# Performance work log

Hardware: AMD Instinct MI355X
Metric: run time of the kernel (lower is better)

## Reference

```python
import jax, jax.numpy as jnp
import numpy as np

DIM = 768
NUM_HEADS = 4
HEAD_DIM = DIM // NUM_HEADS
SCALE = HEAD_DIM ** -0.5


def setup_inputs() -> dict:
    key = jax.random.key(0)
    ks = jax.random.split(key, 8)
    B, N = 8, 2048
    q = jax.random.normal(ks[0], (B, N, DIM), dtype=jnp.float32)
    k = jax.random.normal(ks[1], (B, N, DIM), dtype=jnp.float32)
    v = jax.random.normal(ks[2], (B, N, DIM), dtype=jnp.float32)
    s = DIM ** -0.5
    Wq = jax.random.normal(ks[3], (DIM, DIM), dtype=jnp.float32) * s
    Wk = jax.random.normal(ks[4], (DIM, DIM), dtype=jnp.float32) * s
    Wv = jax.random.normal(ks[5], (DIM, DIM), dtype=jnp.float32) * s
    Wp = jax.random.normal(ks[6], (DIM, DIM), dtype=jnp.float32) * s
    bp = jnp.zeros((DIM,), dtype=jnp.float32)
    return {"q": q, "k": k, "v": v, "Wq": Wq, "Wk": Wk, "Wv": Wv, "Wp": Wp, "bp": bp}


def reference(q, k, v, Wq, Wk, Wv, Wp, bp):
    B, Nq, C = q.shape
    Nk = k.shape[1]
    H, D = NUM_HEADS, HEAD_DIM
    # Linear projections (nn.Linear: x @ W.T), split heads -> [B, H, N, D]
    qh = (q @ Wq.T).reshape(B, Nq, H, D).transpose(0, 2, 1, 3)
    kh = (k @ Wk.T).reshape(B, Nk, H, D).transpose(0, 2, 1, 3)
    vh = (v @ Wv.T).reshape(B, Nk, H, D).transpose(0, 2, 1, 3)
    # Attention scores [B, H, Nq, Nk], softmax over keys
    attn = jnp.einsum('bhqd,bhkd->bhqk', qh, kh) * SCALE
    attn = jax.nn.softmax(attn, axis=-1)
    # Weighted values -> merge heads -> output projection
    x = jnp.einsum('bhqk,bhkd->bhqd', attn, vh)
    x = x.transpose(0, 2, 1, 3).reshape(B, Nq, C)
    return x @ Wp.T + bp
```

## Files before the change

### kernel.cpp

```cpp
#include <hip/hip_runtime.h>
#include <hip/hip_fp16.h>

#define DIMC 768
#define NH 4
#define HD 192
#define SEQ 2048
#define NBATCH 8
#define SCALE_F 0.07216878364870323f
#define LOG2E   1.4426950408889634f
#define DEFER_THR 8.0f

typedef _Float16 f16x8 __attribute__((ext_vector_type(8)));
typedef _Float16 f16x4 __attribute__((ext_vector_type(4)));
typedef float    f32x4 __attribute__((ext_vector_type(4)));

__device__ __forceinline__ f32x4 mfma16(f16x8 a, f16x8 b, f32x4 c) {
    return __builtin_amdgcn_mfma_f32_16x16x32_f16(a, b, c, 0, 0, 0);
}
__device__ __forceinline__ void gl16(const void* g, void* l) {
    __builtin_amdgcn_global_load_lds(
        (const __attribute__((address_space(1))) unsigned int*)g,
        (__attribute__((address_space(3))) unsigned int*)l, 16, 0, 0);
}
__device__ __forceinline__ float exp2_hw(float x) {
    return __builtin_amdgcn_exp2f(x);
}

__global__ __launch_bounds__(256)
void cvt_w(const float* __restrict__ w0, const float* __restrict__ w1,
           const float* __restrict__ w2, const float* __restrict__ w3,
           _Float16* __restrict__ o0, _Float16* __restrict__ o1,
           _Float16* __restrict__ o2, _Float16* __restrict__ o3)
{
    const float* src = (blockIdx.y == 0) ? w0 : (blockIdx.y == 1) ? w1
                     : (blockIdx.y == 2) ? w2 : w3;
    _Float16* dst = (blockIdx.y == 0) ? o0 : (blockIdx.y == 1) ? o1
                  : (blockIdx.y == 2) ? o2 : o3;
    const int e   = blockIdx.x * 256 + threadIdx.x;
    const int row = e / 192;
    const int col = (e - row * 192) * 4;
    const float4 v = *(const float4*)(src + (size_t)row * DIMC + col);
    const int nt = row >> 8, rr = row & 255, t = col >> 6, cc = col & 63;
    f16x4 h = {(_Float16)v.x, (_Float16)v.y, (_Float16)v.z, (_Float16)v.w};
    *(f16x4*)(dst + ((size_t)(nt * 12 + t) * 256 + rr) * 64 + (cc ^ ((rr & 7) << 3))) = h;
}

__device__ __forceinline__ void phase_reads(const _Float16* As, const _Float16* Bs,
                                            int wr, int wc, int l15, int l4, int q,
                                            f16x8 af[2][2], f16x8 bf[2][4], bool loadB)
{
    #pragma unroll
    for (int ks = 0; ks < 2; ++ks) {
        const int cb = ks * 32 + l4 * 8;
        #pragma unroll
        for (int mm = 0; mm < 2; ++mm) {
            const int row = wr * 128 + (q * 2 + mm) * 16 + l15;
            af[ks][mm] = *(const f16x8*)(As + (size_t)row * 64 + (cb ^ ((row & 7) << 3)));
        }
        if (loadB) {
            #pragma unroll
            for (int n = 0; n < 4; ++n) {
                const int row = wc * 64 + n * 16 + l15;
                bf[ks][n] = *(const f16x8*)(Bs + (size_t)row * 64 + (cb ^ ((row & 7) << 3)));
            }
        }
    }
}
__device__ __forceinline__ void phase_mfma(int q, f16x8 af[2][2], f16x8 bf[2][4],
                                           f32x4 acc[8][4])
{
    __builtin_amdgcn_s_barrier();
    asm volatile("s_waitcnt lgkmcnt(0)" ::: "memory");
    __builtin_amdgcn_s_setprio(1);
    #pragma unroll
    for (int ks = 0; ks < 2; ++ks)
        #pragma unroll
        for (int mm = 0; mm < 2; ++mm)
            #pragma unroll
            for (int n = 0; n < 4; ++n)
                acc[q * 2 + mm][n] = mfma16(af[ks][mm], bf[ks][n], acc[q * 2 + mm][n]);
    __builtin_amdgcn_s_setprio(0);
}

template<int MODE>
__global__ __launch_bounds__(512, 2)
void gemm_p8(const float* __restrict__ A, const _Float16* __restrict__ Wimg,
             _Float16* __restrict__ Y, float scale)
{
    __shared__ __attribute__((aligned(16))) _Float16 Abuf[2][16384];
    __shared__ __attribute__((aligned(16))) _Float16 Bbuf[2][16384];

    const int tid  = threadIdx.x;
    const int wid  = tid >> 6;
    const int lane = tid & 63;
    const int l15  = lane & 15;
    const int l4   = lane >> 4;
    const int wr   = wid >> 2;
    const int wc   = wid & 3;
    const int m0   = blockIdx.x * 256;
    const int nt   = blockIdx.y;

    const unsigned char* Wt = (const unsigned char*)(Wimg + (size_t)nt * 12 * 16384);

    f32x4 acc[8][4];
    #pragma unroll
    for (int m = 0; m < 8; ++m)
        #pragma unroll
        for (int n = 0; n < 4; ++n)
            acc[m][n] = (f32x4){0.f, 0.f, 0.f, 0.f};

    float4 rA[8];
    auto loadA = [&](int t) {
        #pragma unroll
        for (int p = 0; p < 8; ++p) {
            const int linear = p * 512 + tid;
            const int row = linear >> 4, qc = (linear & 15) * 4;
            rA[p] = *(const float4*)(A + (size_t)(m0 + row) * DIMC + t * 64 + qc);
        }
    };
    auto writeA = [&](int buf) {
        #pragma unroll
        for (int p = 0; p < 8; ++p) {
            const int linear = p * 512 + tid;
            const int row = linear >> 4, qc = (linear & 15) * 4;
            f16x4 h = {(_Float16)rA[p].x, (_Float16)rA[p].y,
                       (_Float16)rA[p].z, (_Float16)rA[p].w};
            *(f16x4*)(&Abuf[buf][row * 64 + (qc ^ ((row & 7) << 3))]) = h;
        }
    };
    auto stageB = [&](int t) {
        const unsigned char* src = Wt + (size_t)t * 32768;
        #pragma unroll
        for (int u = 0; u < 4; ++u)
            gl16(src + u * 8192 + tid * 16, &Bbuf[t & 1][u * 4096 + tid * 8]);
    };

    loadA(0);
    stageB(0);
    asm volatile("s_waitcnt vmcnt(4)" ::: "memory");
    writeA(0);
    loadA(1);
    asm volatile("s_waitcnt vmcnt(8)" ::: "memory");
    asm volatile("s_waitcnt lgkmcnt(0)" ::: "memory");
    __builtin_amdgcn_s_barrier();

    for (int t = 0; t < 12; ++t) {
        const _Float16* As = &Abuf[t & 1][0];
        const _Float16* Bs = &Bbuf[t & 1][0];
        f16x8 af[2][2], bf[2][4];

        phase_reads(As, Bs, wr, wc, l15, l4, 0, af, bf, true);
        if (t < 11) stageB(t + 1);
        phase_mfma(0, af, bf, acc);
        __builtin_amdgcn_s_barrier();

        phase_reads(As, Bs, wr, wc, l15, l4, 1, af, bf, false);
        phase_mfma(1, af, bf, acc);
        __builtin_amdgcn_s_barrier();

        phase_reads(As, Bs, wr, wc, l15, l4, 2, af, bf, false);
        if (t < 11) {
            asm volatile("s_waitcnt vmcnt(4)" ::: "memory");
            writeA((t + 1) & 1);
            if (t < 10) loadA(t + 2);
        }
        phase_mfma(2, af, bf, acc);
        __builtin_amdgcn_s_barrier();

        phase_reads(As, Bs, wr, wc, l15, l4, 3, af, bf, false);
        phase_mfma(3, af, bf, acc);
        if (t < 10)      asm volatile("s_waitcnt vmcnt(8)" ::: "memory");
        else if (t == 10) asm volatile("s_waitcnt vmcnt(0)" ::: "memory");
        __builtin_amdgcn_s_barrier();
    }

    #pragma unroll
    for (int m = 0; m < 8; ++m) {
        const int rbase = m0 + wr * 128 + m * 16 + l4 * 4;
        #pragma unroll
        for (int n = 0; n < 4; ++n) {
            const int c = nt * 256 + wc * 64 + n * 16 + l15;
            const int h = c / HD;
            const int d = c - h * HD;
            #pragma unroll
            for (int j = 0; j < 4; ++j) {
                const int r  = rbase + j;
                const int b  = r >> 11;
                const int nn = r & (SEQ - 1);
                size_t idx;
                if (MODE == 0) {
                    idx = ((size_t)(b * NH + h) * SEQ + nn) * HD + d;
                } else {
                    const int kt  = nn >> 5;
                    const int key = nn & 31;
                    const size_t tb = ((size_t)(b * NH + h) * 64 + kt) * 12288;
                    if (MODE == 1)
                        idx = tb + (size_t)key * HD + (d ^ ((key & 7) << 3));
                    else
                        idx = tb + 6144 + (((size_t)(key >> 3) * 192 + d) << 3) + (key & 7);
                }
                Y[idx] = (_Float16)(acc[m][n][j] * scale);
            }
        }
    }
}

__global__ __launch_bounds__(512, 2)
void gemm_x8(const _Float16* __restrict__ Ximg, const _Float16* __restrict__ Wimg,
             float* __restrict__ out, const float* __restrict__ bias)
{
    __shared__ __attribute__((aligned(16))) _Float16 Abuf[2][16384];
    __shared__ __attribute__((aligned(16))) _Float16 Bbuf[2][16384];

    const int tid  = threadIdx.x;
    const int wid  = tid >> 6;
    const int lane = tid & 63;
    const int l15  = lane & 15;
    const int l4   = lane >> 4;
    const int wr   = wid >> 2;
    const int wc   = wid & 3;
    const int mt   = blockIdx.x;
    const int nt   = blockIdx.y;

    const unsigned char* Xt = (const unsigned char*)(Ximg + (size_t)mt * 12 * 16384);
    const unsigned char* Wt = (const unsigned char*)(Wimg + (size_t)nt * 12 * 16384);

    f32x4 acc[8][4];
    #pragma unroll
    for (int m = 0; m < 8; ++m)
        #pragma unroll
        for (int n = 0; n < 4; ++n)
            acc[m][n] = (f32x4){0.f, 0.f, 0.f, 0.f};

    auto stageAB = [&](int t) {
        const unsigned char* sa = Xt + (size_t)t * 32768;
        const unsigned char* sb = Wt + (size_t)t * 32768;
        #pragma unroll
        for (int u = 0; u < 4; ++u) {
            gl16(sa + u * 8192 + tid * 16, &Abuf[t & 1][u * 4096 + tid * 8]);
            gl16(sb + u * 8192 + tid * 16, &Bbuf[t & 1][u * 4096 + tid * 8]);
        }
    };

    stageAB(0);
    asm volatile("s_waitcnt vmcnt(0)" ::: "memory");
    __builtin_amdgcn_s_barrier();

    for (int t = 0; t < 12; ++t) {
        const _Float16* As = &Abuf[t & 1][0];
        const _Float16* Bs = &Bbuf[t & 1][0];
        f16x8 af[2][2], bf[2][4];

        phase_reads(As, Bs, wr, wc, l15, l4, 0, af, bf, true);
        if (t < 11) stageAB(t + 1);
        phase_mfma(0, af, bf, acc);
        __builtin_amdgcn_s_barrier();

        phase_reads(As, Bs, wr, wc, l15, l4, 1, af, bf, false);
        phase_mfma(1, af, bf, acc);
        __builtin_amdgcn_s_barrier();

        phase_reads(As, Bs, wr, wc, l15, l4, 2, af, bf, false);
        phase_mfma(2, af, bf, acc);
        __builtin_amdgcn_s_barrier();

        phase_reads(As, Bs, wr, wc, l15, l4, 3, af, bf, false);
        phase_mfma(3, af, bf, acc);
        if (t < 11) asm volatile("s_waitcnt vmcnt(0)" ::: "memory");
        __builtin_amdgcn_s_barrier();
    }

    #pragma unroll
    for (int m = 0; m < 8; ++m) {
        const int rbase = mt * 256 + wr * 128 + m * 16 + l4 * 4;
        #pragma unroll
        for (int n = 0; n < 4; ++n) {
            const int c = nt * 256 + wc * 64 + n * 16 + l15;
            const float bv = bias[c];
            #pragma unroll
            for (int j = 0; j < 4; ++j)
                out[(size_t)(rbase + j) * DIMC + c] = acc[m][n][j] + bv;
        }
    }
}

__global__ __launch_bounds__(512, 4)
void attn7(const _Float16* __restrict__ Qh, const _Float16* __restrict__ KVimg,
           _Float16* __restrict__ Ximg)
{
    __shared__ __attribute__((aligned(16))) _Float16 KV[2][12288];
    __shared__ __attribute__((aligned(16))) _Float16 Ps[8][16][40];

    const int tid  = threadIdx.x;
    const int wid  = tid >> 6;
    const int lane = tid & 63;
    const int l15  = lane & 15;
    const int l4   = lane >> 4;

    const int bid   = blockIdx.x;
    const int local = bid >> 3;
    const int bh    = (bid & 7) * 4 + (local >> 4);
    const int qt    = local & 15;

    const unsigned char* KVt = (const unsigned char*)KVimg + (size_t)bh * 64 * 24576;

    #pragma unroll
    for (int s = 0; s < 3; ++s)
        gl16(KVt + (size_t)(s * 512 + tid) * 16, &KV[0][(size_t)(s * 512 + tid) * 8]);

    const int q0 = qt * 128 + wid * 16;
    const size_t qbase = (size_t)bh * SEQ * HD;
    f16x8 qf[6];
    #pragma unroll
    for (int kk = 0; kk < 6; ++kk)
        qf[kk] = *(const f16x8*)(Qh + qbase + (size_t)(q0 + l15) * HD + kk * 32 + l4 * 8);

    f32x4 Oacc[12];
    #pragma unroll
    for (int nd = 0; nd < 12; ++nd)
        Oacc[nd] = (f32x4){0.f, 0.f, 0.f, 0.f};
    float mrow[4], lrow[4];
    #pragma unroll
    for (int j = 0; j < 4; ++j) { mrow[j] = -1e30f; lrow[j] = 0.f; }

    for (int kt = 0; kt < SEQ / 32; ++kt) {
        const int cur = kt & 1;
        if (kt < SEQ / 32 - 1) {
            const unsigned char* KVn = KVt + (size_t)(kt + 1) * 24576;
            #pragma unroll
            for (int s = 0; s < 3; ++s)
                gl16(KVn + (size_t)(s * 512 + tid) * 16,
                     &KV[cur ^ 1][(size_t)(s * 512 + tid) * 8]);
            asm volatile("s_waitcnt vmcnt(3)" ::: "memory");
        } else {
            asm volatile("s_waitcnt vmcnt(0)" ::: "memory");
        }
        __builtin_amdgcn_s_barrier();
        __builtin_amdgcn_sched_barrier(0);

        const _Float16* Kc = &KV[cur][0];
        const _Float16* Vc = &KV[cur][6144];

        f32x4 sacc[2];
        sacc[0] = (f32x4){0.f, 0.f, 0.f, 0.f};
        sacc[1] = (f32x4){0.f, 0.f, 0.f, 0.f};
        __builtin_amdgcn_s_setprio(1);
        #pragma unroll
        for (int kk = 0; kk < 6; ++kk) {
            const int cb = (kk * 32 + l4 * 8) ^ ((l15 & 7) << 3);
            #pragma unroll
            for (int nn = 0; nn < 2; ++nn) {
                const f16x8 kf = *(const f16x8*)(Kc + (size_t)(nn * 16 + l15) * HD + cb);
                sacc[nn] = mfma16(qf[kk], kf, sacc[nn]);
            }
        }
        __builtin_amdgcn_s_setprio(0);

        float lm[4];
        bool need = false;
        #pragma unroll
        for (int j = 0; j < 4; ++j) {
            lm[j] = fmaxf(sacc[0][j], sacc[1][j]);
            need |= (lm[j] > mrow[j] + DEFER_THR);
        }
        if (__any(need)) {
            #pragma unroll
            for (int j = 0; j < 4; ++j) {
                float v = lm[j];
                v = fmaxf(v, __shfl_xor(v, 1));
                v = fmaxf(v, __shfl_xor(v, 2));
                v = fmaxf(v, __shfl_xor(v, 4));
                v = fmaxf(v, __shfl_xor(v, 8));
                const float mnew = fmaxf(mrow[j], v);
                const float f    = exp2_hw(mrow[j] - mnew);
                mrow[j] = mnew;
                lrow[j] *= f;
                #pragma unroll
                for (int nd = 0; nd < 12; ++nd)
                    Oacc[nd][j] *= f;
            }
        }
        #pragma unroll
        for (int j = 0; j < 4; ++j) {
            const float p0 = exp2_hw(sacc[0][j] - mrow[j]);
            const float p1 = exp2_hw(sacc[1][j] - mrow[j]);
            sacc[0][j] = p0;
            sacc[1][j] = p1;
            lrow[j] += p0 + p1;
        }

        #pragma unroll
        for (int nn = 0; nn < 2; ++nn)
            #pragma unroll
            for (int j = 0; j < 4; ++j)
                Ps[wid][l4 * 4 + j][nn * 16 + l15] = (_Float16)sacc[nn][j];
        asm volatile("s_waitcnt lgkmcnt(0)" ::: "memory");
        __builtin_amdgcn_sched_barrier(0);

        const f16x8 pf = *(const f16x8*)(&Ps[wid][l15][l4 * 8]);
        __builtin_amdgcn_s_setprio(1);
        #pragma unroll
        for (int nd = 0; nd < 12; ++nd) {
            const f16x8 vfr = *(const f16x8*)(Vc + (((size_t)l4 * 192 + nd * 16 + l15) << 3));
            Oacc[nd] = mfma16(pf, vfr, Oacc[nd]);
        }
        __builtin_amdgcn_s_setprio(0);

        __builtin_amdgcn_s_barrier();
        __builtin_amdgcn_sched_barrier(0);
    }

    #pragma unroll
    for (int j = 0; j < 4; ++j) {
        float s = lrow[j];
        s += __shfl_xor(s, 1);
        s += __shfl_xor(s, 2);
        s += __shfl_xor(s, 4);
        s += __shfl_xor(s, 8);
        lrow[j] = s;
    }
    const int b = bh >> 2;
    const int h = bh & 3;
    #pragma unroll
    for (int j = 0; j < 4; ++j) {
        const float inv = 1.f / lrow[j];
        const int qrow = q0 + l4 * 4 + j;
        const int gr   = b * SEQ + qrow;
        const int mt   = gr >> 8;
        const int rr   = gr & 255;
        #pragma unroll
        for (int nd = 0; nd < 12; ++nd) {
            const int gc = h * HD + nd * 16 + l15;
            const int t  = gc >> 6;
            const int cc = gc & 63;
            Ximg[((size_t)(mt * 12 + t) * 256 + rr) * 64 + (cc ^ ((rr & 7) << 3))] =
                (_Float16)(Oacc[nd][j] * inv);
        }
    }
}

extern "C" void kernel_launch(void* const* d_in, const int* in_sizes, int n_in,
                              void* d_out, int out_size, void* d_ws, size_t ws_size,
                              hipStream_t stream)
{
    const float* q  = (const float*)d_in[0];
    const float* k  = (const float*)d_in[1];
    const float* v  = (const float*)d_in[2];
    const float* Wq = (const float*)d_in[3];
    const float* Wk = (const float*)d_in[4];
    const float* Wv = (const float*)d_in[5];
    const float* Wp = (const float*)d_in[6];
    const float* bp = (const float*)d_in[7];

    const size_t HSZ  = (size_t)NBATCH * NH * SEQ * HD;
    const size_t WIMG = 3 * 12 * 16384;
    _Float16* Qh    = (_Float16*)d_ws;
    _Float16* KVimg = Qh + HSZ;
    _Float16* Ximg  = KVimg + 2 * HSZ;
    _Float16* Wpimg = Ximg + HSZ;
    _Float16* Wqimg = (_Float16*)d_out;
    _Float16* Wkimg = Wqimg + WIMG;
    _Float16* Wvimg = Wkimg + WIMG;

    cvt_w<<<dim3(576, 4), dim3(256), 0, stream>>>(Wq, Wk, Wv, Wp,
                                                  Wqimg, Wkimg, Wvimg, Wpimg);
    dim3 g8(64, 3), b8(512);
    gemm_p8<0><<<g8, b8, 0, stream>>>(q, Wqimg, Qh, SCALE_F * LOG2E);
    gemm_p8<1><<<g8, b8, 0, stream>>>(k, Wkimg, KVimg, 1.0f);
    gemm_p8<3><<<g8, b8, 0, stream>>>(v, Wvimg, KVimg, 1.0f);
    attn7<<<dim3(512), dim3(512), 0, stream>>>(Qh, KVimg, Ximg);
    gemm_x8<<<g8, b8, 0, stream>>>(Ximg, Wpimg, (float*)d_out, bp);
}
```

Before: 262.8 us.

## Merge Q/K/V projection GEMMs into one launch and unroll attention K/V double buffer

Replaces three separate projection GEMM launches with a single 64x9 grid kernel that picks the q/k/v input, weight slice and output layout from blockIdx.y. This gives one larger wave of blocks that can fill the GPU better and removes two launch gaps and their tails. The attention kernel now splits the K/V double buffer into two named LDS arrays and unrolls the tile loop by two, so buffer addresses are static instead of computed from kt&1. The merged kernel adds runtime branches in the epilogue, and a leftover unused gemm_qkv kernel is also added.

```diff
diff --git a/kernel.cpp b/kernel.cpp
--- a/kernel.cpp
+++ b/kernel.cpp
@@ -82,10 +82,9 @@
     __builtin_amdgcn_s_setprio(0);
 }
 
-template<int MODE>
 __global__ __launch_bounds__(512, 2)
-void gemm_p8(const float* __restrict__ A, const _Float16* __restrict__ Wimg,
-             _Float16* __restrict__ Y, float scale)
+void gemm_qkv(const float* __restrict__ A, const _Float16* __restrict__ Wimg,
+              _Float16* __restrict__ Qh, _Float16* __restrict__ KVimg, float qs)
 {
     __shared__ __attribute__((aligned(16))) _Float16 Abuf[2][16384];
     __shared__ __attribute__((aligned(16))) _Float16 Bbuf[2][16384];
@@ -99,6 +98,9 @@
     const int wc   = wid & 3;
     const int m0   = blockIdx.x * 256;
     const int nt   = blockIdx.y;
+    const int which = nt / 3;
+    const int sub   = nt - which * 3;
+    const float scale = (which == 0) ? qs : 1.0f;
 
     const unsigned char* Wt = (const unsigned char*)(Wimg + (size_t)nt * 12 * 16384);
 
@@ -108,6 +110,8 @@
         #pragma unroll
         for (int n = 0; n < 4; ++n)
             acc[m][n] = (f32x4){0.f, 0.f, 0.f, 0.f};
+
+    const float* Asrc = A + (size_t)which * (16384ull * DIMC);
 
     float4 rA[8];
     auto loadA = [&](int t) {
@@ -115,7 +119,7 @@
         for (int p = 0; p < 8; ++p) {
             const int linear = p * 512 + tid;
             const int row = linear >> 4, qc = (linear & 15) * 4;
-            rA[p] = *(const float4*)(A + (size_t)(m0 + row) * DIMC + t * 64 + qc);
+            rA[p] = *(const float4*)(Asrc + (size_t)(m0 + row) * DIMC + t * 64 + qc);
         }
     };
     auto writeA = [&](int buf) {
@@ -169,7 +173,7 @@
 
         phase_reads(As, Bs, wr, wc, l15, l4, 3, af, bf, false);
         phase_mfma(3, af, bf, acc);
-        if (t < 10)      asm volatile("s_waitcnt vmcnt(8)" ::: "memory");
+        if (t < 10)       asm volatile("s_waitcnt vmcnt(8)" ::: "memory");
         else if (t == 10) asm volatile("s_waitcnt vmcnt(0)" ::: "memory");
         __builtin_amdgcn_s_barrier();
     }
@@ -179,7 +183,7 @@
         const int rbase = m0 + wr * 128 + m * 16 + l4 * 4;
         #pragma unroll
         for (int n = 0; n < 4; ++n) {
-            const int c = nt * 256 + wc * 64 + n * 16 + l15;
+            const int c = sub * 256 + wc * 64 + n * 16 + l15;
             const int h = c / HD;
             const int d = c - h * HD;
             #pragma unroll
@@ -187,19 +191,20 @@
                 const int r  = rbase + j;
                 const int b  = r >> 11;
                 const int nn = r & (SEQ - 1);
-                size_t idx;
-                if (MODE == 0) {
-                    idx = ((size_t)(b * NH + h) * SEQ + nn) * HD + d;
+                if (which == 0) {
+                    Qh[((size_t)(b * NH + h) * SEQ + nn) * HD + d] =
+                        (_Float16)(acc[m][n][j] * scale);
                 } else {
                     const int kt  = nn >> 5;
                     const int key = nn & 31;
                     const size_t tb = ((size_t)(b * NH + h) * 64 + kt) * 12288;
-                    if (MODE == 1)
+                    size_t idx;
+                    if (which == 1)
                         idx = tb + (size_t)key * HD + (d ^ ((key & 7) << 3));
                     else
                         idx = tb + 6144 + (((size_t)(key >> 3) * 192 + d) << 3) + (key & 7);
+                    KVimg[idx] = (_Float16)acc[m][n][j];
                 }
-                Y[idx] = (_Float16)(acc[m][n][j] * scale);
             }
         }
     }
@@ -285,10 +290,11 @@
 }
 
 __global__ __launch_bounds__(512, 4)
-void attn7(const _Float16* __restrict__ Qh, const _Float16* __restrict__ KVimg,
+void attn8(const _Float16* __restrict__ Qh, const _Float16* __restrict__ KVimg,
            _Float16* __restrict__ Ximg)
 {
-    __shared__ __attribute__((aligned(16))) _Float16 KV[2][12288];
+    __shared__ __attribute__((aligned(16))) _Float16 KV0[12288];
+    __shared__ __attribute__((aligned(16))) _Float16 KV1[12288];
     __shared__ __attribute__((aligned(16))) _Float16 Ps[8][16][40];
 
     const int tid  = threadIdx.x;
@@ -304,9 +310,14 @@
 
     const unsigned char* KVt = (const unsigned char*)KVimg + (size_t)bh * 64 * 24576;
 
-    #pragma unroll
-    for (int s = 0; s < 3; ++s)
-        gl16(KVt + (size_t)(s * 512 + tid) * 16, &KV[0][(size_t)(s * 512 + tid) * 8]);
+    auto stage = [&](_Float16* dst, int t) {
+        const unsigned char* src = KVt + (size_t)t * 24576;
+        #pragma unroll
+        for (int s = 0; s < 3; ++s)
+            gl16(src + (size_t)(s * 512 + tid) * 16, dst + (size_t)(s * 512 + tid) * 8);
+    };
+
+    stage(KV0, 0);
 
     const int q0 = qt * 128 + wid * 16;
     const size_t qbase = (size_t)bh * SEQ * HD;
@@ -323,23 +334,16 @@
     #pragma unroll
     for (int j = 0; j < 4; ++j) { mrow[j] = -1e30f; lrow[j] = 0.f; }
 
-    for (int kt = 0; kt < SEQ / 32; ++kt) {
-        const int cur = kt & 1;
-        if (kt < SEQ / 32 - 1) {
-            const unsigned char* KVn = KVt + (size_t)(kt + 1) * 24576;
-            #pragma unroll
-            for (int s = 0; s < 3; ++s)
-                gl16(KVn + (size_t)(s * 512 + tid) * 16,
-                     &KV[cur ^ 1][(size_t)(s * 512 + tid) * 8]);
+    auto iter = [&](const _Float16* Kc, const _Float16* Vc,
+                    _Float16* stageDst, int nextT, bool doStage) {
+        if (doStage) {
+            stage(stageDst, nextT);
             asm volatile("s_waitcnt vmcnt(3)" ::: "memory");
         } else {
             asm volatile("s_waitcnt vmcnt(0)" ::: "memory");
         }
         __builtin_amdgcn_s_barrier();
         __builtin_amdgcn_sched_barrier(0);
-
-        const _Float16* Kc = &KV[cur][0];
-        const _Float16* Vc = &KV[cur][6144];
 
         f32x4 sacc[2];
         sacc[0] = (f32x4){0.f, 0.f, 0.f, 0.f};
@@ -408,6 +412,11 @@
 
         __builtin_amdgcn_s_barrier();
         __builtin_amdgcn_sched_barrier(0);
+    };
+
+    for (int kt = 0; kt < SEQ / 32; kt += 2) {
+        iter(&KV0[0], &KV0[6144], KV1, kt + 1, true);
+        iter(&KV1[0], &KV1[6144], KV0, kt + 2, kt + 2 < SEQ / 32);
     }
 
     #pragma unroll
@@ -464,10 +473,141 @@
 
     cvt_w<<<dim3(576, 4), dim3(256), 0, stream>>>(Wq, Wk, Wv, Wp,
                                                   Wqimg, Wkimg, Wvimg, Wpimg);
-    dim3 g8(64, 3), b8(512);
-    gemm_p8<0><<<g8, b8, 0, stream>>>(q, Wqimg, Qh, SCALE_F * LOG2E);
-    gemm_p8<1><<<g8, b8, 0, stream>>>(k, Wkimg, KVimg, 1.0f);
-    gemm_p8<3><<<g8, b8, 0, stream>>>(v, Wvimg, KVimg, 1.0f);
-    attn7<<<dim3(512), dim3(512), 0, stream>>>(Qh, KVimg, Ximg);
-    gemm_x8<<<g8, b8, 0, stream>>>(Ximg, Wpimg, (float*)d_out, bp);
-}
+    (void)0;
+    {
+        extern __global__ void gemm_qkv3(const float*, const float*, const float*,
+                                         const _Float16*, _Float16*, _Float16*, float);
+        gemm_qkv3<<<dim3(64, 9), dim3(512), 0, stream>>>(q, k, v, Wqimg, Qh, KVimg,
+                                                         SCALE_F * LOG2E);
+    }
+    attn8<<<dim3(512), dim3(512), 0, stream>>>(Qh, KVimg, Ximg);
+    gemm_x8<<<dim3(64, 3), dim3(512), 0, stream>>>(Ximg, Wpimg, (float*)d_out, bp);
+}
+
+__global__ __launch_bounds__(512, 2)
+void gemm_qkv3(const float* __restrict__ qA, const float* __restrict__ kA,
+               const float* __restrict__ vA, const _Float16* __restrict__ Wimg,
+               _Float16* __restrict__ Qh, _Float16* __restrict__ KVimg, float qs)
+{
+    __shared__ __attribute__((aligned(16))) _Float16 Abuf[2][16384];
+    __shared__ __attribute__((aligned(16))) _Float16 Bbuf[2][16384];
+
+    const int tid  = threadIdx.x;
+    const int wid  = tid >> 6;
+    const int lane = tid & 63;
+    const int l15  = lane & 15;
+    const int l4   = lane >> 4;
+    const int wr   = wid >> 2;
+    const int wc   = wid & 3;
+    const int m0   = blockIdx.x * 256;
+    const int nt   = blockIdx.y;
+    const int which = nt / 3;
+    const int sub   = nt - which * 3;
+
+    const float* Asrc = (which == 0) ? qA : (which == 1) ? kA : vA;
+    const unsigned char* Wt = (const unsigned char*)(Wimg + (size_t)nt * 12 * 16384);
+
+    f32x4 acc[8][4];
+    #pragma unroll
+    for (int m = 0; m < 8; ++m)
+        #pragma unroll
+        for (int n = 0; n < 4; ++n)
+            acc[m][n] = (f32x4){0.f, 0.f, 0.f, 0.f};
+
+    float4 rA[8];
+    auto loadA = [&](int t) {
+        #pragma unroll
+        for (int p = 0; p < 8; ++p) {
+            const int linear = p * 512 + tid;
+            const int row = linear >> 4, qc = (linear & 15) * 4;
+            rA[p] = *(const float4*)(Asrc + (size_t)(m0 + row) * DIMC + t * 64 + qc);
+        }
+    };
+    auto writeA = [&](int buf) {
+        #pragma unroll
+        for (int p = 0; p < 8; ++p) {
+            const int linear = p * 512 + tid;
+            const int row = linear >> 4, qc = (linear & 15) * 4;
+            f16x4 h = {(_Float16)rA[p].x, (_Float16)rA[p].y,
+                       (_Float16)rA[p].z, (_Float16)rA[p].w};
+            *(f16x4*)(&Abuf[buf][row * 64 + (qc ^ ((row & 7) << 3))]) = h;
+        }
+    };
+    auto stageB = [&](int t) {
+        const unsigned char* src = Wt + (size_t)t * 32768;
+        #pragma unroll
+        for (int u = 0; u < 4; ++u)
+            gl16(src + u * 8192 + tid * 16, &Bbuf[t & 1][u * 4096 + tid * 8]);
+    };
+
+    loadA(0);
+    stageB(0);
+    asm volatile("s_waitcnt vmcnt(4)" ::: "memory");
+    writeA(0);
+    loadA(1);
+    asm volatile("s_waitcnt vmcnt(8)" ::: "memory");
+    asm volatile("s_waitcnt lgkmcnt(0)" ::: "memory");
+    __builtin_amdgcn_s_barrier();
+
+    for (int t = 0; t < 12; ++t) {
+        const _Float16* As = &Abuf[t & 1][0];
+        const _Float16* Bs = &Bbuf[t & 1][0];
+        f16x8 af[2][2], bf[2][4];
+
+        phase_reads(As, Bs, wr, wc, l15, l4, 0, af, bf, true);
+        if (t < 11) stageB(t + 1);
+        phase_mfma(0, af, bf, acc);
+        __builtin_amdgcn_s_barrier();
+
+        phase_reads(As, Bs, wr, wc, l15, l4, 1, af, bf, false);
+        phase_mfma(1, af, bf, acc);
+        __builtin_amdgcn_s_barrier();
+
+        phase_reads(As, Bs, wr, wc, l15, l4, 2, af, bf, false);
+        if (t < 11) {
+            asm volatile("s_waitcnt vmcnt(4)" ::: "memory");
+            writeA((t + 1) & 1);
+            if (t < 10) loadA(t + 2);
+        }
+        phase_mfma(2, af, bf, acc);
+        __builtin_amdgcn_s_barrier();
+
+        phase_reads(As, Bs, wr, wc, l15, l4, 3, af, bf, false);
+        phase_mfma(3, af, bf, acc);
+        if (t < 10)       asm volatile("s_waitcnt vmcnt(8)" ::: "memory");
+        else if (t == 10) asm volatile("s_waitcnt vmcnt(0)" ::: "memory");
+        __builtin_amdgcn_s_barrier();
+    }
+
+    const float scale = (which == 0) ? qs : 1.0f;
+    #pragma unroll
+    for (int m = 0; m < 8; ++m) {
+        const int rbase = m0 + wr * 128 + m * 16 + l4 * 4;
+        #pragma unroll
+        for (int n = 0; n < 4; ++n) {
+            const int c = sub * 256 + wc * 64 + n * 16 + l15;
+            const int h = c / HD;
+            const int d = c - h * HD;
+            #pragma unroll
+            for (int j = 0; j < 4; ++j) {
+                const int r  = rbase + j;
+                const int b  = r >> 11;
+                const int nn = r & (SEQ - 1);
+                if (which == 0) {
+                    Qh[((size_t)(b * NH + h) * SEQ + nn) * HD + d] =
+                        (_Float16)(acc[m][n][j] * scale);
+                } else {
+                    const int kt  = nn >> 5;
+                    const int key = nn & 31;
+                    const size_t tb = ((size_t)(b * NH + h) * 64 + kt) * 12288;
+                    size_t idx;
+                    if (which == 1)
+                        idx = tb + (size_t)key * HD + (d ^ ((key & 7) << 3));
+                    else
+                        idx = tb + 6144 + (((size_t)(key >> 3) * 192 + d) << 3) + (key & 7);
+                    KVimg[idx] = (_Float16)acc[m][n][j];
+                }
+            }
+        }
+    }
+}
```

New measurement: 270.6 us. 3.0% more time.

## Switch projection GEMMs to 16-wave blocks and unroll attention double buffer

Applied to the files above, without the earlier changes.

The projection and output GEMMs move from 8-wave blocks with a four-phase ping-pong schedule to 1024-thread blocks. Each wave now owns a 64x64 sub-tile and runs a single simpler compute step per k-tile, which lowers per-wave register pressure. Staging of B and A is reordered behind full vmcnt(0) waits, which may cut load/compute overlap. The attention kernel gets two named LDS buffers and a loop unrolled by two, so buffer addresses become compile-time constants.

```diff
diff --git a/kernel.cpp b/kernel.cpp
--- a/kernel.cpp
+++ b/kernel.cpp
@@ -45,47 +45,36 @@
     *(f16x4*)(dst + ((size_t)(nt * 12 + t) * 256 + rr) * 64 + (cc ^ ((rr & 7) << 3))) = h;
 }
 
-__device__ __forceinline__ void phase_reads(const _Float16* As, const _Float16* Bs,
-                                            int wr, int wc, int l15, int l4, int q,
-                                            f16x8 af[2][2], f16x8 bf[2][4], bool loadB)
+__device__ __forceinline__ void tile_compute(const _Float16* As, const _Float16* Bs,
+                                             int wr, int wc, int l15, int l4,
+                                             f32x4 acc[4][4])
 {
     #pragma unroll
     for (int ks = 0; ks < 2; ++ks) {
         const int cb = ks * 32 + l4 * 8;
-        #pragma unroll
-        for (int mm = 0; mm < 2; ++mm) {
-            const int row = wr * 128 + (q * 2 + mm) * 16 + l15;
-            af[ks][mm] = *(const f16x8*)(As + (size_t)row * 64 + (cb ^ ((row & 7) << 3)));
-        }
-        if (loadB) {
-            #pragma unroll
-            for (int n = 0; n < 4; ++n) {
-                const int row = wc * 64 + n * 16 + l15;
-                bf[ks][n] = *(const f16x8*)(Bs + (size_t)row * 64 + (cb ^ ((row & 7) << 3)));
-            }
-        }
-    }
-}
-__device__ __forceinline__ void phase_mfma(int q, f16x8 af[2][2], f16x8 bf[2][4],
-                                           f32x4 acc[8][4])
-{
-    __builtin_amdgcn_s_barrier();
-    asm volatile("s_waitcnt lgkmcnt(0)" ::: "memory");
-    __builtin_amdgcn_s_setprio(1);
-    #pragma unroll
-    for (int ks = 0; ks < 2; ++ks)
-        #pragma unroll
-        for (int mm = 0; mm < 2; ++mm)
+        f16x8 bf[4];
+        #pragma unroll
+        for (int n = 0; n < 4; ++n) {
+            const int row = wc * 64 + n * 16 + l15;
+            bf[n] = *(const f16x8*)(Bs + (size_t)row * 64 + (cb ^ ((row & 7) << 3)));
+        }
+        __builtin_amdgcn_s_setprio(1);
+        #pragma unroll
+        for (int m = 0; m < 4; ++m) {
+            const int row = wr * 64 + m * 16 + l15;
+            const f16x8 af = *(const f16x8*)(As + (size_t)row * 64 + (cb ^ ((row & 7) << 3)));
             #pragma unroll
             for (int n = 0; n < 4; ++n)
-                acc[q * 2 + mm][n] = mfma16(af[ks][mm], bf[ks][n], acc[q * 2 + mm][n]);
-    __builtin_amdgcn_s_setprio(0);
+                acc[m][n] = mfma16(af, bf[n], acc[m][n]);
+        }
+        __builtin_amdgcn_s_setprio(0);
+    }
 }
 
 template<int MODE>
-__global__ __launch_bounds__(512, 2)
-void gemm_p8(const float* __restrict__ A, const _Float16* __restrict__ Wimg,
-             _Float16* __restrict__ Y, float scale)
+__global__ __launch_bounds__(1024)
+void gemm_p16(const float* __restrict__ A, const _Float16* __restrict__ Wimg,
+              _Float16* __restrict__ Y, float scale)
 {
     __shared__ __attribute__((aligned(16))) _Float16 Abuf[2][16384];
     __shared__ __attribute__((aligned(16))) _Float16 Bbuf[2][16384];
@@ -102,26 +91,26 @@
 
     const unsigned char* Wt = (const unsigned char*)(Wimg + (size_t)nt * 12 * 16384);
 
-    f32x4 acc[8][4];
-    #pragma unroll
-    for (int m = 0; m < 8; ++m)
+    f32x4 acc[4][4];
+    #pragma unroll
+    for (int m = 0; m < 4; ++m)
         #pragma unroll
         for (int n = 0; n < 4; ++n)
             acc[m][n] = (f32x4){0.f, 0.f, 0.f, 0.f};
 
-    float4 rA[8];
+    float4 rA[4];
     auto loadA = [&](int t) {
         #pragma unroll
-        for (int p = 0; p < 8; ++p) {
-            const int linear = p * 512 + tid;
+        for (int p = 0; p < 4; ++p) {
+            const int linear = p * 1024 + tid;
             const int row = linear >> 4, qc = (linear & 15) * 4;
             rA[p] = *(const float4*)(A + (size_t)(m0 + row) * DIMC + t * 64 + qc);
         }
     };
     auto writeA = [&](int buf) {
         #pragma unroll
-        for (int p = 0; p < 8; ++p) {
-            const int linear = p * 512 + tid;
+        for (int p = 0; p < 4; ++p) {
+            const int linear = p * 1024 + tid;
             const int row = linear >> 4, qc = (linear & 15) * 4;
             f16x4 h = {(_Float16)rA[p].x, (_Float16)rA[p].y,
                        (_Float16)rA[p].z, (_Float16)rA[p].w};
@@ -131,52 +120,40 @@
     auto stageB = [&](int t) {
         const unsigned char* src = Wt + (size_t)t * 32768;
         #pragma unroll
-        for (int u = 0; u < 4; ++u)
-            gl16(src + u * 8192 + tid * 16, &Bbuf[t & 1][u * 4096 + tid * 8]);
-    };
-
+        for (int u = 0; u < 2; ++u)
+            gl16(src + u * 16384 + tid * 16, &Bbuf[t & 1][u * 8192 + tid * 8]);
+    };
+
+    stageB(0);
     loadA(0);
-    stageB(0);
-    asm volatile("s_waitcnt vmcnt(4)" ::: "memory");
+    asm volatile("s_waitcnt vmcnt(0)" ::: "memory");
     writeA(0);
     loadA(1);
-    asm volatile("s_waitcnt vmcnt(8)" ::: "memory");
     asm volatile("s_waitcnt lgkmcnt(0)" ::: "memory");
     __builtin_amdgcn_s_barrier();
 
     for (int t = 0; t < 12; ++t) {
         const _Float16* As = &Abuf[t & 1][0];
         const _Float16* Bs = &Bbuf[t & 1][0];
-        f16x8 af[2][2], bf[2][4];
-
-        phase_reads(As, Bs, wr, wc, l15, l4, 0, af, bf, true);
-        if (t < 11) stageB(t + 1);
-        phase_mfma(0, af, bf, acc);
-        __builtin_amdgcn_s_barrier();
-
-        phase_reads(As, Bs, wr, wc, l15, l4, 1, af, bf, false);
-        phase_mfma(1, af, bf, acc);
-        __builtin_amdgcn_s_barrier();
-
-        phase_reads(As, Bs, wr, wc, l15, l4, 2, af, bf, false);
+
         if (t < 11) {
-            asm volatile("s_waitcnt vmcnt(4)" ::: "memory");
+            asm volatile("s_waitcnt vmcnt(0)" ::: "memory");
+            stageB(t + 1);
             writeA((t + 1) & 1);
             if (t < 10) loadA(t + 2);
         }
-        phase_mfma(2, af, bf, acc);
+
+        tile_compute(As, Bs, wr, wc, l15, l4, acc);
+
+        if (t < 10)       asm volatile("s_waitcnt vmcnt(4)" ::: "memory");
+        else if (t == 10) asm volatile("s_waitcnt vmcnt(0)" ::: "memory");
+        asm volatile("s_waitcnt lgkmcnt(0)" ::: "memory");
         __builtin_amdgcn_s_barrier();
-
-        phase_reads(As, Bs, wr, wc, l15, l4, 3, af, bf, false);
-        phase_mfma(3, af, bf, acc);
-        if (t < 10)      asm volatile("s_waitcnt vmcnt(8)" ::: "memory");
-        else if (t == 10) asm volatile("s_waitcnt vmcnt(0)" ::: "memory");
-        __builtin_amdgcn_s_barrier();
-    }
-
-    #pragma unroll
-    for (int m = 0; m < 8; ++m) {
-        const int rbase = m0 + wr * 128 + m * 16 + l4 * 4;
+    }
+
+    #pragma unroll
+    for (int m = 0; m < 4; ++m) {
+        const int rbase = m0 + wr * 64 + m * 16 + l4 * 4;
         #pragma unroll
         for (int n = 0; n < 4; ++n) {
             const int c = nt * 256 + wc * 64 + n * 16 + l15;
@@ -187,27 +164,28 @@
                 const int r  = rbase + j;
                 const int b  = r >> 11;
                 const int nn = r & (SEQ - 1);
-                size_t idx;
                 if (MODE == 0) {
-                    idx = ((size_t)(b * NH + h) * SEQ + nn) * HD + d;
+                    Y[((size_t)(b * NH + h) * SEQ + nn) * HD + d] =
+                        (_Float16)(acc[m][n][j] * scale);
                 } else {
                     const int kt  = nn >> 5;
                     const int key = nn & 31;
                     const size_t tb = ((size_t)(b * NH + h) * 64 + kt) * 12288;
+                    size_t idx;
                     if (MODE == 1)
                         idx = tb + (size_t)key * HD + (d ^ ((key & 7) << 3));
                     else
                         idx = tb + 6144 + (((size_t)(key >> 3) * 192 + d) << 3) + (key & 7);
+                    Y[idx] = (_Float16)acc[m][n][j];
                 }
-                Y[idx] = (_Float16)(acc[m][n][j] * scale);
             }
         }
     }
 }
 
-__global__ __launch_bounds__(512, 2)
-void gemm_x8(const _Float16* __restrict__ Ximg, const _Float16* __restrict__ Wimg,
-             float* __restrict__ out, const float* __restrict__ bias)
+__global__ __launch_bounds__(1024)
+void gemm_x16(const _Float16* __restrict__ Ximg, const _Float16* __restrict__ Wimg,
+              float* __restrict__ out, const float* __restrict__ bias)
 {
     __shared__ __attribute__((aligned(16))) _Float16 Abuf[2][16384];
     __shared__ __attribute__((aligned(16))) _Float16 Bbuf[2][16384];
@@ -225,9 +203,9 @@
     const unsigned char* Xt = (const unsigned char*)(Ximg + (size_t)mt * 12 * 16384);
     const unsigned char* Wt = (const unsigned char*)(Wimg + (size_t)nt * 12 * 16384);
 
-    f32x4 acc[8][4];
-    #pragma unroll
-    for (int m = 0; m < 8; ++m)
+    f32x4 acc[4][4];
+    #pragma unroll
+    for (int m = 0; m < 4; ++m)
         #pragma unroll
         for (int n = 0; n < 4; ++n)
             acc[m][n] = (f32x4){0.f, 0.f, 0.f, 0.f};
@@ -236,9 +214,9 @@
         const unsigned char* sa = Xt + (size_t)t * 32768;
         const unsigned char* sb = Wt + (size_t)t * 32768;
         #pragma unroll
-        for (int u = 0; u < 4; ++u) {
-            gl16(sa + u * 8192 + tid * 16, &Abuf[t & 1][u * 4096 + tid * 8]);
-            gl16(sb + u * 8192 + tid * 16, &Bbuf[t & 1][u * 4096 + tid * 8]);
+        for (int u = 0; u < 2; ++u) {
+            gl16(sa + u * 16384 + tid * 16, &Abuf[t & 1][u * 8192 + tid * 8]);
+            gl16(sb + u * 16384 + tid * 16, &Bbuf[t & 1][u * 8192 + tid * 8]);
         }
     };
 
@@ -249,30 +227,18 @@
     for (int t = 0; t < 12; ++t) {
         const _Float16* As = &Abuf[t & 1][0];
         const _Float16* Bs = &Bbuf[t & 1][0];
-        f16x8 af[2][2], bf[2][4];
-
-        phase_reads(As, Bs, wr, wc, l15, l4, 0, af, bf, true);
+
         if (t < 11) stageAB(t + 1);
-        phase_mfma(0, af, bf, acc);
-        __builtin_amdgcn_s_barrier();
-
-        phase_reads(As, Bs, wr, wc, l15, l4, 1, af, bf, false);
-        phase_mfma(1, af, bf, acc);
-        __builtin_amdgcn_s_barrier();
-
-        phase_reads(As, Bs, wr, wc, l15, l4, 2, af, bf, false);
-        phase_mfma(2, af, bf, acc);
-        __builtin_amdgcn_s_barrier();
-
-        phase_reads(As, Bs, wr, wc, l15, l4, 3, af, bf, false);
-        phase_mfma(3, af, bf, acc);
+
+        tile_compute(As, Bs, wr, wc, l15, l4, acc);
+
         if (t < 11) asm volatile("s_waitcnt vmcnt(0)" ::: "memory");
         __builtin_amdgcn_s_barrier();
     }
 
     #pragma unroll
-    for (int m = 0; m < 8; ++m) {
-        const int rbase = mt * 256 + wr * 128 + m * 16 + l4 * 4;
+    for (int m = 0; m < 4; ++m) {
+        const int rbase = mt * 256 + wr * 64 + m * 16 + l4 * 4;
         #pragma unroll
         for (int n = 0; n < 4; ++n) {
             const int c = nt * 256 + wc * 64 + n * 16 + l15;
@@ -285,10 +251,11 @@
 }
 
 __global__ __launch_bounds__(512, 4)
-void attn7(const _Float16* __restrict__ Qh, const _Float16* __restrict__ KVimg,
+void attn8(const _Float16* __restrict__ Qh, const _Float16* __restrict__ KVimg,
            _Float16* __restrict__ Ximg)
 {
-    __shared__ __attribute__((aligned(16))) _Float16 KV[2][12288];
+    __shared__ __attribute__((aligned(16))) _Float16 KV0[12288];
+    __shared__ __attribute__((aligned(16))) _Float16 KV1[12288];
     __shared__ __attribute__((aligned(16))) _Float16 Ps[8][16][40];
 
     const int tid  = threadIdx.x;
@@ -304,9 +271,14 @@
 
     const unsigned char* KVt = (const unsigned char*)KVimg + (size_t)bh * 64 * 24576;
 
-    #pragma unroll
-    for (int s = 0; s < 3; ++s)
-        gl16(KVt + (size_t)(s * 512 + tid) * 16, &KV[0][(size_t)(s * 512 + tid) * 8]);
+    auto stage = [&](_Float16* dst, int t) {
+        const unsigned char* src = KVt + (size_t)t * 24576;
+        #pragma unroll
+        for (int s = 0; s < 3; ++s)
+            gl16(src + (size_t)(s * 512 + tid) * 16, dst + (size_t)(s * 512 + tid) * 8);
+    };
+
+    stage(KV0, 0);
 
     const int q0 = qt * 128 + wid * 16;
     const size_t qbase = (size_t)bh * SEQ * HD;
@@ -323,23 +295,16 @@
     #pragma unroll
     for (int j = 0; j < 4; ++j) { mrow[j] = -1e30f; lrow[j] = 0.f; }
 
-    for (int kt = 0; kt < SEQ / 32; ++kt) {
-        const int cur = kt & 1;
-        if (kt < SEQ / 32 - 1) {
-            const unsigned char* KVn = KVt + (size_t)(kt + 1) * 24576;
-            #pragma unroll
-            for (int s = 0; s < 3; ++s)
-                gl16(KVn + (size_t)(s * 512 + tid) * 16,
-                     &KV[cur ^ 1][(size_t)(s * 512 + tid) * 8]);
+    auto iter = [&](const _Float16* Kc, const _Float16* Vc,
+                    _Float16* stageDst, int nextT, bool doStage) {
+        if (doStage) {
+            stage(stageDst, nextT);
             asm volatile("s_waitcnt vmcnt(3)" ::: "memory");
         } else {
             asm volatile("s_waitcnt vmcnt(0)" ::: "memory");
         }
         __builtin_amdgcn_s_barrier();
         __builtin_amdgcn_sched_barrier(0);
-
-        const _Float16* Kc = &KV[cur][0];
-        const _Float16* Vc = &KV[cur][6144];
 
         f32x4 sacc[2];
         sacc[0] = (f32x4){0.f, 0.f, 0.f, 0.f};
@@ -408,6 +373,11 @@
 
         __builtin_amdgcn_s_barrier();
         __builtin_amdgcn_sched_barrier(0);
+    };
+
+    for (int kt = 0; kt < SEQ / 32; kt += 2) {
+        iter(&KV0[0], &KV0[6144], KV1, kt + 1, true);
+        iter(&KV1[0], &KV1[6144], KV0, kt + 2, kt + 2 < SEQ / 32);
     }
 
     #pragma unroll
@@ -464,10 +434,10 @@
 
     cvt_w<<<dim3(576, 4), dim3(256), 0, stream>>>(Wq, Wk, Wv, Wp,
                                                   Wqimg, Wkimg, Wvimg, Wpimg);
-    dim3 g8(64, 3), b8(512);
-    gemm_p8<0><<<g8, b8, 0, stream>>>(q, Wqimg, Qh, SCALE_F * LOG2E);
-    gemm_p8<1><<<g8, b8, 0, stream>>>(k, Wkimg, KVimg, 1.0f);
-    gemm_p8<3><<<g8, b8, 0, stream>>>(v, Wvimg, KVimg, 1.0f);
-    attn7<<<dim3(512), dim3(512), 0, stream>>>(Qh, KVimg, Ximg);
-    gemm_x8<<<g8, b8, 0, stream>>>(Ximg, Wpimg, (float*)d_out, bp);
-}
+    dim3 g16(64, 3), b16(1024);
+    gemm_p16<0><<<g16, b16, 0, stream>>>(q, Wqimg, Qh, SCALE_F * LOG2E);
+    gemm_p16<1><<<g16, b16, 0, stream>>>(k, Wkimg, KVimg, 1.0f);
+    gemm_p16<3><<<g16, b16, 0, stream>>>(v, Wvimg, KVimg, 1.0f);
+    attn8<<<dim3(512), dim3(512), 0, stream>>>(Qh, KVimg, Ximg);
+    gemm_x16<<<g16, b16, 0, stream>>>(Ximg, Wpimg, (float*)d_out, bp);
+}
```

Result: slower. 282.2 us (+7.4%).
